# Kernel tuning notes

Hardware: AMD Instinct MI355X
Metric: run time of the kernel (lower is better)

## Reference

```python
import jax, jax.numpy as jnp
import numpy as np

N_NODES = 50000
N_EDGES = 800000
D_IN = 128
H1 = H2 = H3 = 128
N_CLASS = 16
N_GRAPHS = 500


def setup_inputs() -> dict:
    key = jax.random.key(0)
    ks = jax.random.split(key, 10)
    x = jax.random.normal(ks[0], (N_NODES, D_IN), dtype=jnp.float32)
    edge_src = jax.random.randint(ks[1], (N_EDGES,), 0, N_NODES)
    edge_dst = jax.random.randint(ks[2], (N_EDGES,), 0, N_NODES)
    idx = jnp.sort(jax.random.randint(ks[3], (N_NODES,), 0, N_GRAPHS))
    s = 0.02  # small init scale
    W1 = jax.random.normal(ks[4], (D_IN, H1), dtype=jnp.float32) * s
    W2 = jax.random.normal(ks[5], (H1, H2), dtype=jnp.float32) * s
    W3 = jax.random.normal(ks[6], (H2, H3), dtype=jnp.float32) * s
    W4 = jax.random.normal(ks[7], (H3, N_CLASS), dtype=jnp.float32) * s
    b1 = jnp.zeros((H1,), jnp.float32)
    b2 = jnp.zeros((H2,), jnp.float32)
    b3 = jnp.zeros((H3,), jnp.float32)
    b4 = jnp.zeros((N_CLASS,), jnp.float32)
    return {"x": x, "edge_src": edge_src, "edge_dst": edge_dst, "idx": idx,
            "W1": W1, "b1": b1, "W2": W2, "b2": b2,
            "W3": W3, "b3": b3, "W4": W4, "b4": b4}


def reference(x, edge_src, edge_dst, idx, W1, b1, W2, b2, W3, b3, W4, b4):
    # adj_tilde @ h  with binary adjacency + identity, in edge-list form:
    # row i accumulates h[j] for every edge (i<-j), plus h[i] from the eye.
    def propagate(h):
        return h + jax.ops.segment_sum(h[edge_src], edge_dst, num_segments=h.shape[0])

    z1 = jax.nn.relu(propagate(x) @ W1 + b1)            # [N, H1]
    h = propagate(z1) @ W2 + b2                          # [N, H2]
    # scatter_add pooling per graph id (fixed number of graphs for jit)
    pooled = jax.ops.segment_sum(h, idx, num_segments=N_GRAPHS)  # [G, H2]
    zg = jax.nn.relu(pooled @ W3 + b3)                   # [G, H3]
    out = zg @ W4 + b4                                   # [G, C]
    return jax.nn.log_softmax(out, axis=1)
```

## Files before the change

### kernel.cpp

```cpp
#include <hip/hip_runtime.h>
#include <hip/hip_bf16.h>
#include <math.h>

#define NN 50000
#define NE 800000
#define DD 128
#define NG 500
#define NC 16

#define BBITS 6
#define BDSTS 64
#define NBK ((NN + BDSTS - 1) / BDSTS)
#define NCHUNK 256
#define EPB (NE / NCHUNK)
#define ECAP 1536
#define NSLICE 4
#define GEMMBLK ((NN + 127) / 128)

using short8 = __attribute__((ext_vector_type(8))) short;
using f32x4  = __attribute__((ext_vector_type(4))) float;

static __device__ __forceinline__ ushort f2bf(float f) {
    __hip_bfloat16 h = __float2bfloat16(f);
    ushort r;
    __builtin_memcpy(&r, &h, sizeof(r));
    return r;
}
static __device__ __forceinline__ float bflo(uint v) { return __uint_as_float(v << 16); }
static __device__ __forceinline__ float bfhi(uint v) { return __uint_as_float(v & 0xffff0000u); }
static __device__ __forceinline__ uint packbf(float lo, float hi) {
    return ((uint)f2bf(hi) << 16) | (uint)f2bf(lo);
}

static __device__ __forceinline__ void add8(float* acc, uint4 v) {
    acc[0] += bflo(v.x); acc[1] += bfhi(v.x);
    acc[2] += bflo(v.y); acc[3] += bfhi(v.y);
    acc[4] += bflo(v.z); acc[5] += bfhi(v.z);
    acc[6] += bflo(v.w); acc[7] += bfhi(v.w);
}

static __device__ __forceinline__ int lower_bound_idx(const int* __restrict__ idx, int g) {
    if (g >= NG) return NN;
    int lo = 0, hi = NN;
    while (lo < hi) {
        int mid = (lo + hi) >> 1;
        if (idx[mid] < g) lo = mid + 1; else hi = mid;
    }
    return lo;
}

static __device__ __forceinline__ int chunk_of_block(int blk) {
    return (blk & 7) * 32 + (blk >> 3);
}

__global__ __launch_bounds__(256) void k0_count_convert_kernel(const int* __restrict__ edst,
                                                               int* __restrict__ cnt,
                                                               const float* __restrict__ W1,
                                                               ushort* __restrict__ W1t) {
    int t = threadIdx.x;
    if (blockIdx.x < NCHUNK) {
        __shared__ int hist[NBK];
        int chunk = chunk_of_block(blockIdx.x);
        const int e0 = chunk * EPB;
        for (int b = t; b < NBK; b += 256) hist[b] = 0;
        __syncthreads();
        for (int i = t; i < EPB; i += 256) atomicAdd(&hist[edst[e0 + i] >> BBITS], 1);
        __syncthreads();
        for (int b = t; b < NBK; b += 256) cnt[(size_t)chunk * NBK + b] = hist[b];
    } else {
        int flat = (blockIdx.x - NCHUNK) * 256 + t;
        if (flat < 128 * 128) {
            int k = flat >> 7, n = flat & 127;
            W1t[n * 128 + k] = f2bf(W1[flat]);
        }
    }
}

static __device__ __forceinline__ void gemm_body(int blk, int tid,
                                                 const float* __restrict__ X,
                                                 const ushort* __restrict__ W1t,
                                                 ushort* __restrict__ Y, int M) {
    const int wave = tid >> 6, lane = tid & 63;
    const int wm = wave >> 1, wn = wave & 1;
    const int m0 = blk * 128 + wm * 64;
    const int n0 = wn * 64;
    const int lr = lane & 15;
    const int lk = (lane >> 4) * 8;

    int rows[4];
    bool valid[4];
    #pragma unroll
    for (int m = 0; m < 4; ++m) {
        rows[m] = m0 + m * 16 + lr;
        valid[m] = rows[m] < M;
    }

    f32x4 acc[4][4] = {};

    #pragma unroll
    for (int kc = 0; kc < 4; ++kc) {
        const int kb = kc * 32 + lk;
        short8 a[4];
        #pragma unroll
        for (int m = 0; m < 4; ++m) {
            union { short8 v; ushort u[8]; } ua;
            if (valid[m]) {
                const float* p = &X[(size_t)rows[m] * 128 + kb];
                float4 v0 = *reinterpret_cast<const float4*>(p);
                float4 v1 = *reinterpret_cast<const float4*>(p + 4);
                ua.u[0] = f2bf(v0.x); ua.u[1] = f2bf(v0.y);
                ua.u[2] = f2bf(v0.z); ua.u[3] = f2bf(v0.w);
                ua.u[4] = f2bf(v1.x); ua.u[5] = f2bf(v1.y);
                ua.u[6] = f2bf(v1.z); ua.u[7] = f2bf(v1.w);
            } else {
                #pragma unroll
                for (int j = 0; j < 8; ++j) ua.u[j] = 0;
            }
            a[m] = ua.v;
        }
        short8 b[4];
        #pragma unroll
        for (int n = 0; n < 4; ++n) {
            b[n] = *reinterpret_cast<const short8*>(&W1t[(size_t)(n0 + n * 16 + lr) * 128 + kb]);
        }
        #pragma unroll
        for (int m = 0; m < 4; ++m)
            #pragma unroll
            for (int n = 0; n < 4; ++n)
                acc[m][n] = __builtin_amdgcn_mfma_f32_16x16x32_bf16(a[m], b[n], acc[m][n], 0, 0, 0);
    }

    const int rbase = (lane >> 4) * 4;
    #pragma unroll
    for (int m = 0; m < 4; ++m) {
        #pragma unroll
        for (int r = 0; r < 4; ++r) {
            int row = m0 + m * 16 + rbase + r;
            if (row < M) {
                #pragma unroll
                for (int n = 0; n < 4; ++n) {
                    Y[(size_t)row * 128 + n0 + n * 16 + lr] = f2bf(acc[m][n][r]);
                }
            }
        }
    }
}

__global__ __launch_bounds__(256) void k1_gemm_scan1_kernel(const float* __restrict__ X,
                                                            const ushort* __restrict__ W1t,
                                                            ushort* __restrict__ Y,
                                                            const int* __restrict__ cnt,
                                                            int* __restrict__ bpos,
                                                            int* __restrict__ btot) {
    if (blockIdx.x < GEMMBLK) {
        gemm_body(blockIdx.x, threadIdx.x, X, W1t, Y, NN);
    } else {
        __shared__ int s[256];
        int b = blockIdx.x - GEMMBLK, t = threadIdx.x;
        int v = cnt[(size_t)t * NBK + b];
        s[t] = v;
        __syncthreads();
        for (int d = 1; d < 256; d <<= 1) {
            int x = (t >= d) ? s[t - d] : 0;
            __syncthreads();
            s[t] += x;
            __syncthreads();
        }
        bpos[b * NCHUNK + t] = s[t] - v;
        if (t == 255) btot[b] = s[255];
    }
}

__global__ __launch_bounds__(1024) void csr_scan2_kernel(const int* __restrict__ btot,
                                                         int* __restrict__ bbase) {
    __shared__ int s[1024];
    int t = threadIdx.x;
    int v = (t < NBK) ? btot[t] : 0;
    s[t] = v;
    __syncthreads();
    for (int d = 1; d < 1024; d <<= 1) {
        int x = (t >= d) ? s[t - d] : 0;
        __syncthreads();
        s[t] += x;
        __syncthreads();
    }
    if (t < NBK) bbase[t] = s[t] - v;
}

__global__ __launch_bounds__(256) void csr_scatter_kernel(const int* __restrict__ esrc,
                                                          const int* __restrict__ edst,
                                                          const int* __restrict__ bbase,
                                                          const int* __restrict__ bpos,
                                                          uint* __restrict__ baux) {
    __shared__ int lbase[NBK];
    __shared__ int cur[NBK];
    int t = threadIdx.x;
    int chunk = chunk_of_block(blockIdx.x);
    const int e0 = chunk * EPB;
    for (int b = t; b < NBK; b += 256) {
        lbase[b] = bbase[b] + bpos[b * NCHUNK + chunk];
        cur[b] = 0;
    }
    __syncthreads();
    for (int i = t; i < EPB; i += 256) {
        int d = edst[e0 + i], s = esrc[e0 + i];
        int b = d >> BBITS;
        int r = atomicAdd(&cur[b], 1);
        baux[lbase[b] + r] = ((uint)(d & (BDSTS - 1)) << 16) | (uint)s;
    }
}

__global__ __launch_bounds__(256) void bucket_sort_kernel(const uint* __restrict__ baux,
                                                          const int* __restrict__ btot,
                                                          const int* __restrict__ bbase,
                                                          int* __restrict__ offsets,
                                                          ushort* __restrict__ csr) {
    __shared__ uint ent[ECAP];
    __shared__ int hist[BDSTS], lofs[BDSTS], cur[BDSTS];
    int b = blockIdx.x, t = threadIdx.x;
    int n = btot[b];
    int base = bbase[b];
    if (t < BDSTS) hist[t] = 0;
    __syncthreads();
    for (int i = t; i < n; i += 256) {
        uint e = baux[base + i];
        ent[i] = e;
        atomicAdd(&hist[e >> 16], 1);
    }
    __syncthreads();
    if (t < BDSTS) lofs[t] = hist[t];
    __syncthreads();
    for (int d = 1; d < BDSTS; d <<= 1) {
        int x = 0;
        if (t < BDSTS && t >= d) x = lofs[t - d];
        __syncthreads();
        if (t < BDSTS) lofs[t] += x;
        __syncthreads();
    }
    int d0 = b * BDSTS;
    if (t < BDSTS) {
        int excl = lofs[t] - hist[t];
        lofs[t] = excl;
        cur[t] = 0;
        if (d0 + t < NN) offsets[d0 + t] = base + excl;
    }
    if (b == NBK - 1 && t == 0) offsets[NN] = NE;
    __syncthreads();
    for (int i = t; i < n; i += 256) {
        uint e = ent[i];
        int j = e >> 16;
        int pos = base + lofs[j] + atomicAdd(&cur[j], 1);
        csr[pos] = (ushort)(e & 0xffffu);
    }
}

__global__ __launch_bounds__(256) void prop1_kernel(const ushort* __restrict__ In,
                                                    const int* __restrict__ offs,
                                                    const ushort* __restrict__ csr,
                                                    const float* __restrict__ bias,
                                                    ushort* __restrict__ Out, int n) {
    int node = (blockIdx.x * blockDim.x + threadIdx.x) >> 6;
    int lane = threadIdx.x & 63;
    if (node >= n) return;
    const int q = lane >> 4;
    const int p = lane & 15;
    const uint4* Ir = reinterpret_cast<const uint4*>(In);

    float acc[8] = {};
    if (q == 0) add8(acc, Ir[(size_t)node * 16 + p]);

    int e = offs[node] + q, e1 = offs[node + 1];
    for (; e + 12 < e1; e += 16) {
        int s0 = csr[e], s1 = csr[e + 4], s2 = csr[e + 8], s3 = csr[e + 12];
        uint4 v0 = Ir[(size_t)s0 * 16 + p];
        uint4 v1 = Ir[(size_t)s1 * 16 + p];
        uint4 v2 = Ir[(size_t)s2 * 16 + p];
        uint4 v3 = Ir[(size_t)s3 * 16 + p];
        add8(acc, v0); add8(acc, v1); add8(acc, v2); add8(acc, v3);
    }
    for (; e < e1; e += 4) add8(acc, Ir[(size_t)csr[e] * 16 + p]);

    #pragma unroll
    for (int j = 0; j < 8; ++j) {
        acc[j] += __shfl_xor(acc[j], 16);
        acc[j] += __shfl_xor(acc[j], 32);
    }

    if (q == 0) {
        float4 bA = *reinterpret_cast<const float4*>(&bias[p * 8]);
        float4 bB = *reinterpret_cast<const float4*>(&bias[p * 8 + 4]);
        uint4 o;
        o.x = packbf(fmaxf(acc[0] + bA.x, 0.f), fmaxf(acc[1] + bA.y, 0.f));
        o.y = packbf(fmaxf(acc[2] + bA.z, 0.f), fmaxf(acc[3] + bA.w, 0.f));
        o.z = packbf(fmaxf(acc[4] + bB.x, 0.f), fmaxf(acc[5] + bB.y, 0.f));
        o.w = packbf(fmaxf(acc[6] + bB.z, 0.f), fmaxf(acc[7] + bB.w, 0.f));
        reinterpret_cast<uint4*>(Out)[(size_t)node * 16 + p] = o;
    }
}

__global__ __launch_bounds__(256) void prop2pool_kernel(const ushort* __restrict__ Z1,
                                                        const int* __restrict__ offs,
                                                        const ushort* __restrict__ csr,
                                                        const int* __restrict__ idx,
                                                        float* __restrict__ partials) {
    int g = blockIdx.x >> 2, s = blockIdx.x & (NSLICE - 1);
    int gs = lower_bound_idx(idx, g);
    int ge = lower_bound_idx(idx, g + 1);
    int w = threadIdx.x >> 6, lane = threadIdx.x & 63;
    int q = lane >> 4, p = lane & 15;
    int stream = s * 16 + w * 4 + q;
    const uint4* Zr = reinterpret_cast<const uint4*>(Z1);

    float acc[8] = {};
    for (int i = gs + stream; i < ge; i += 64) add8(acc, Zr[(size_t)i * 16 + p]);
    int E0 = offs[gs], E1 = offs[ge];
    int e = E0 + stream;
    for (; e + 192 < E1; e += 256) {
        int s0 = csr[e], s1 = csr[e + 64], s2 = csr[e + 128], s3 = csr[e + 192];
        uint4 v0 = Zr[(size_t)s0 * 16 + p];
        uint4 v1 = Zr[(size_t)s1 * 16 + p];
        uint4 v2 = Zr[(size_t)s2 * 16 + p];
        uint4 v3 = Zr[(size_t)s3 * 16 + p];
        add8(acc, v0); add8(acc, v1); add8(acc, v2); add8(acc, v3);
    }
    for (; e < E1; e += 64) add8(acc, Zr[(size_t)csr[e] * 16 + p]);

    #pragma unroll
    for (int j = 0; j < 8; ++j) {
        acc[j] += __shfl_xor(acc[j], 16);
        acc[j] += __shfl_xor(acc[j], 32);
    }
    __shared__ float red[4][128];
    if (q == 0) {
        #pragma unroll
        for (int j = 0; j < 8; ++j) red[w][p * 8 + j] = acc[j];
    }
    __syncthreads();
    int t = threadIdx.x;
    if (t < 128) {
        partials[((size_t)g * NSLICE + s) * 128 + t] =
            red[0][t] + red[1][t] + red[2][t] + red[3][t];
    }
}

__global__ __launch_bounds__(128) void head_kernel(const float* __restrict__ partials,
                                                   const int* __restrict__ idx,
                                                   const float* __restrict__ W2, const float* __restrict__ b2,
                                                   const float* __restrict__ W3, const float* __restrict__ b3,
                                                   const float* __restrict__ W4, const float* __restrict__ b4,
                                                   float* __restrict__ out) {
    int g = blockIdx.x, t = threadIdx.x;
    __shared__ float vs[128], hs[128], zs[128], os[16];
    const float* pp = &partials[(size_t)g * NSLICE * 128];
    vs[t] = pp[t] + pp[128 + t] + pp[256 + t] + pp[384 + t];
    __syncthreads();
    float c = (float)(lower_bound_idx(idx, g + 1) - lower_bound_idx(idx, g));
    float a = c * b2[t];
    #pragma unroll 8
    for (int k = 0; k < 128; ++k) a = fmaf(vs[k], W2[k * 128 + t], a);
    hs[t] = a;
    __syncthreads();
    float z = b3[t];
    #pragma unroll 8
    for (int k = 0; k < 128; ++k) z = fmaf(hs[k], W3[k * 128 + t], z);
    zs[t] = fmaxf(z, 0.f);
    __syncthreads();
    if (t < 16) {
        float oo = b4[t];
        #pragma unroll 8
        for (int k = 0; k < 128; ++k) oo = fmaf(zs[k], W4[k * 16 + t], oo);
        os[t] = oo;
    }
    __syncthreads();
    if (t < 16) {
        float m = -INFINITY;
        #pragma unroll
        for (int k = 0; k < 16; ++k) m = fmaxf(m, os[k]);
        float ssum = 0.f;
        #pragma unroll
        for (int k = 0; k < 16; ++k) ssum += expf(os[k] - m);
        out[g * 16 + t] = os[t] - m - logf(ssum);
    }
}

extern "C" void kernel_launch(void* const* d_in, const int* in_sizes, int n_in,
                              void* d_out, int out_size, void* d_ws, size_t ws_size,
                              hipStream_t stream) {
    const float* x    = (const float*)d_in[0];
    const int*   esrc = (const int*)d_in[1];
    const int*   edst = (const int*)d_in[2];
    const int*   idx  = (const int*)d_in[3];
    const float* W1   = (const float*)d_in[4];
    const float* b1   = (const float*)d_in[5];
    const float* W2   = (const float*)d_in[6];
    const float* b2   = (const float*)d_in[7];
    const float* W3   = (const float*)d_in[8];
    const float* b3   = (const float*)d_in[9];
    const float* W4   = (const float*)d_in[10];
    const float* b4   = (const float*)d_in[11];
    float* out = (float*)d_out;

    char* w = (char*)d_ws;
    auto alloc = [&](size_t bytes) -> void* {
        void* p = (void*)w;
        w += (bytes + 255) & ~(size_t)255;
        return p;
    };
    int* cnt      = (int*)alloc((size_t)NCHUNK * NBK * 4);
    int* bpos     = (int*)alloc((size_t)NBK * NCHUNK * 4);
    int* btot     = (int*)alloc((size_t)NBK * 4);
    int* bbase    = (int*)alloc((size_t)NBK * 4);
    uint* baux    = (uint*)alloc((size_t)NE * 4);
    int* offsets  = (int*)alloc((size_t)(NN + 1) * 4);
    ushort* csr   = (ushort*)alloc((size_t)NE * 2);
    ushort* w1t   = (ushort*)alloc((size_t)DD * DD * 2);
    ushort* y     = (ushort*)alloc((size_t)NN * DD * 2);
    ushort* z1    = (ushort*)alloc((size_t)NN * DD * 2);
    float* partials = (float*)alloc((size_t)NG * NSLICE * DD * 4);

    k0_count_convert_kernel<<<NCHUNK + 64, 256, 0, stream>>>(edst, cnt, W1, w1t);

    k1_gemm_scan1_kernel<<<GEMMBLK + NBK, 256, 0, stream>>>(x, w1t, y, cnt, bpos, btot);

    csr_scan2_kernel<<<1, 1024, 0, stream>>>(btot, bbase);
    csr_scatter_kernel<<<NCHUNK, 256, 0, stream>>>(esrc, edst, bbase, bpos, baux);
    bucket_sort_kernel<<<NBK, 256, 0, stream>>>(baux, btot, bbase, offsets, csr);

    prop1_kernel<<<NN / 4, 256, 0, stream>>>(y, offsets, csr, b1, z1, NN);

    prop2pool_kernel<<<NG * NSLICE, 256, 0, stream>>>(z1, offsets, csr, idx, partials);

    head_kernel<<<NG, 128, 0, stream>>>(partials, idx, W2, b2, W3, b3, W4, b4, out);
}
```

Measured before the change: 127.6 us.

## Fold bucket scan into scatter and fuse pooling with head kernel

Removes the single-block scan kernel: each scatter block now redundantly computes the exclusive scan of bucket totals itself, and block 0 writes bbase for later use. The pooled propagation and the MLP head are merged into one 1024-thread block per graph, dropping the partials buffer and a launch. This removes two launches and their gaps. The cost is redundant scan work in every scatter block, and only 500 large blocks for the gather phase instead of 2000 smaller ones, which may lower occupancy and load balance.

```diff
diff --git a/kernel.cpp b/kernel.cpp
--- a/kernel.cpp
+++ b/kernel.cpp
@@ -14,7 +14,6 @@
 #define NCHUNK 256
 #define EPB (NE / NCHUNK)
 #define ECAP 1536
-#define NSLICE 4
 #define GEMMBLK ((NN + 127) / 128)
 
 using short8 = __attribute__((ext_vector_type(8))) short;
@@ -171,37 +170,49 @@
     }
 }
 
-__global__ __launch_bounds__(1024) void csr_scan2_kernel(const int* __restrict__ btot,
-                                                         int* __restrict__ bbase) {
-    __shared__ int s[1024];
-    int t = threadIdx.x;
-    int v = (t < NBK) ? btot[t] : 0;
-    s[t] = v;
-    __syncthreads();
-    for (int d = 1; d < 1024; d <<= 1) {
-        int x = (t >= d) ? s[t - d] : 0;
-        __syncthreads();
-        s[t] += x;
-        __syncthreads();
-    }
-    if (t < NBK) bbase[t] = s[t] - v;
-}
-
 __global__ __launch_bounds__(256) void csr_scatter_kernel(const int* __restrict__ esrc,
                                                           const int* __restrict__ edst,
-                                                          const int* __restrict__ bbase,
+                                                          const int* __restrict__ btot,
                                                           const int* __restrict__ bpos,
+                                                          int* __restrict__ bbase,
                                                           uint* __restrict__ baux) {
     __shared__ int lbase[NBK];
     __shared__ int cur[NBK];
+    __shared__ int tsA[256], tsB[256];
     int t = threadIdx.x;
     int chunk = chunk_of_block(blockIdx.x);
     const int e0 = chunk * EPB;
-    for (int b = t; b < NBK; b += 256) {
-        lbase[b] = bbase[b] + bpos[b * NCHUNK + chunk];
-        cur[b] = 0;
-    }
-    __syncthreads();
+
+    int loc[4];
+    int sum = 0;
+    #pragma unroll
+    for (int j = 0; j < 4; ++j) {
+        int b = t * 4 + j;
+        loc[j] = (b < NBK) ? btot[b] : 0;
+        sum += loc[j];
+    }
+    tsA[t] = sum;
+    __syncthreads();
+    int* sbuf = tsA;
+    int* dbuf = tsB;
+    for (int d = 1; d < 256; d <<= 1) {
+        dbuf[t] = sbuf[t] + ((t >= d) ? sbuf[t - d] : 0);
+        __syncthreads();
+        int* tmp = sbuf; sbuf = dbuf; dbuf = tmp;
+    }
+    int excl = sbuf[t] - sum;
+    #pragma unroll
+    for (int j = 0; j < 4; ++j) {
+        int b = t * 4 + j;
+        if (b < NBK) {
+            if (blockIdx.x == 0) bbase[b] = excl;
+            lbase[b] = excl + bpos[b * NCHUNK + chunk];
+            cur[b] = 0;
+        }
+        excl += loc[j];
+    }
+    __syncthreads();
+
     for (int i = t; i < EPB; i += 256) {
         int d = edst[e0 + i], s = esrc[e0 + i];
         int b = d >> BBITS;
@@ -298,17 +309,20 @@
     }
 }
 
-__global__ __launch_bounds__(256) void prop2pool_kernel(const ushort* __restrict__ Z1,
-                                                        const int* __restrict__ offs,
-                                                        const ushort* __restrict__ csr,
-                                                        const int* __restrict__ idx,
-                                                        float* __restrict__ partials) {
-    int g = blockIdx.x >> 2, s = blockIdx.x & (NSLICE - 1);
+__global__ __launch_bounds__(1024) void prop2head_kernel(const ushort* __restrict__ Z1,
+                                                         const int* __restrict__ offs,
+                                                         const ushort* __restrict__ csr,
+                                                         const int* __restrict__ idx,
+                                                         const float* __restrict__ W2, const float* __restrict__ b2,
+                                                         const float* __restrict__ W3, const float* __restrict__ b3,
+                                                         const float* __restrict__ W4, const float* __restrict__ b4,
+                                                         float* __restrict__ out) {
+    int g = blockIdx.x, t = threadIdx.x;
     int gs = lower_bound_idx(idx, g);
     int ge = lower_bound_idx(idx, g + 1);
-    int w = threadIdx.x >> 6, lane = threadIdx.x & 63;
+    int w = t >> 6, lane = t & 63;
     int q = lane >> 4, p = lane & 15;
-    int stream = s * 16 + w * 4 + q;
+    int stream = w * 4 + q;
     const uint4* Zr = reinterpret_cast<const uint4*>(Z1);
 
     float acc[8] = {};
@@ -330,40 +344,35 @@
         acc[j] += __shfl_xor(acc[j], 16);
         acc[j] += __shfl_xor(acc[j], 32);
     }
-    __shared__ float red[4][128];
+    __shared__ float red[16][128];
     if (q == 0) {
         #pragma unroll
         for (int j = 0; j < 8; ++j) red[w][p * 8 + j] = acc[j];
     }
     __syncthreads();
-    int t = threadIdx.x;
+
+    __shared__ float vs[128], hs[128], zs[128], os[16];
     if (t < 128) {
-        partials[((size_t)g * NSLICE + s) * 128 + t] =
-            red[0][t] + red[1][t] + red[2][t] + red[3][t];
-    }
-}
-
-__global__ __launch_bounds__(128) void head_kernel(const float* __restrict__ partials,
-                                                   const int* __restrict__ idx,
-                                                   const float* __restrict__ W2, const float* __restrict__ b2,
-                                                   const float* __restrict__ W3, const float* __restrict__ b3,
-                                                   const float* __restrict__ W4, const float* __restrict__ b4,
-                                                   float* __restrict__ out) {
-    int g = blockIdx.x, t = threadIdx.x;
-    __shared__ float vs[128], hs[128], zs[128], os[16];
-    const float* pp = &partials[(size_t)g * NSLICE * 128];
-    vs[t] = pp[t] + pp[128 + t] + pp[256 + t] + pp[384 + t];
-    __syncthreads();
-    float c = (float)(lower_bound_idx(idx, g + 1) - lower_bound_idx(idx, g));
-    float a = c * b2[t];
-    #pragma unroll 8
-    for (int k = 0; k < 128; ++k) a = fmaf(vs[k], W2[k * 128 + t], a);
-    hs[t] = a;
-    __syncthreads();
-    float z = b3[t];
-    #pragma unroll 8
-    for (int k = 0; k < 128; ++k) z = fmaf(hs[k], W3[k * 128 + t], z);
-    zs[t] = fmaxf(z, 0.f);
+        float s = 0.f;
+        #pragma unroll
+        for (int k = 0; k < 16; ++k) s += red[k][t];
+        vs[t] = s;
+    }
+    __syncthreads();
+    if (t < 128) {
+        float c = (float)(ge - gs);
+        float a = c * b2[t];
+        #pragma unroll 8
+        for (int k = 0; k < 128; ++k) a = fmaf(vs[k], W2[k * 128 + t], a);
+        hs[t] = a;
+    }
+    __syncthreads();
+    if (t < 128) {
+        float z = b3[t];
+        #pragma unroll 8
+        for (int k = 0; k < 128; ++k) z = fmaf(hs[k], W3[k * 128 + t], z);
+        zs[t] = fmaxf(z, 0.f);
+    }
     __syncthreads();
     if (t < 16) {
         float oo = b4[t];
@@ -416,19 +425,16 @@
     ushort* w1t   = (ushort*)alloc((size_t)DD * DD * 2);
     ushort* y     = (ushort*)alloc((size_t)NN * DD * 2);
     ushort* z1    = (ushort*)alloc((size_t)NN * DD * 2);
-    float* partials = (float*)alloc((size_t)NG * NSLICE * DD * 4);
 
     k0_count_convert_kernel<<<NCHUNK + 64, 256, 0, stream>>>(edst, cnt, W1, w1t);
 
     k1_gemm_scan1_kernel<<<GEMMBLK + NBK, 256, 0, stream>>>(x, w1t, y, cnt, bpos, btot);
 
-    csr_scan2_kernel<<<1, 1024, 0, stream>>>(btot, bbase);
-    csr_scatter_kernel<<<NCHUNK, 256, 0, stream>>>(esrc, edst, bbase, bpos, baux);
+    csr_scatter_kernel<<<NCHUNK, 256, 0, stream>>>(esrc, edst, btot, bpos, bbase, baux);
     bucket_sort_kernel<<<NBK, 256, 0, stream>>>(baux, btot, bbase, offsets, csr);
 
     prop1_kernel<<<NN / 4, 256, 0, stream>>>(y, offsets, csr, b1, z1, NN);
 
-    prop2pool_kernel<<<NG * NSLICE, 256, 0, stream>>>(z1, offsets, csr, idx, partials);
-
-    head_kernel<<<NG, 128, 0, stream>>>(partials, idx, W2, b2, W3, b3, W4, b4, out);
-}
+    prop2head_kernel<<<NG, 1024, 0, stream>>>(z1, offsets, csr, idx,
+                                              W2, b2, W3, b3, W4, b4, out);
+}
```

After: 113.7 us. -10.9%, faster.
